# Optimization experiments

Hardware: AMD Instinct MI355X
Metric: run time of the kernel (lower is better)

The kernel has to match this reference:

```python
import jax, jax.numpy as jnp
import numpy as np

D_MODEL = 2048
SEQ_LEN = 16   # R is built for context_window=16 in the original module
BATCH = 256


def make_rotary_matrix(m, d):
    # Faithful to get_rotary_matrix: theta = 10000 ** (-2*(i-1)/d)  (note the i-1 bug kept)
    pos = np.arange(m, dtype=np.float64)[:, None]            # [m,1]
    i = np.arange(d // 2, dtype=np.float64)[None, :]         # [1,d/2]
    theta = 10000.0 ** (-2.0 * (i - 1.0) / d)
    ang = pos * theta                                         # [m, d/2]
    cos, sin = np.cos(ang), np.sin(ang)
    R = np.zeros((m, d, d), dtype=np.float32)
    idx = np.arange(d // 2)
    R[:, 2 * idx, 2 * idx] = cos
    R[:, 2 * idx, 2 * idx + 1] = -sin
    R[:, 2 * idx + 1, 2 * idx] = sin
    R[:, 2 * idx + 1, 2 * idx + 1] = cos
    return jnp.asarray(R)


def setup_inputs() -> dict:
    key = jax.random.key(0)
    kx, kq, kk, kv = jax.random.split(key, 4)
    s = 1.0 / np.sqrt(D_MODEL)
    return {
        "x": jax.random.normal(kx, (BATCH, SEQ_LEN, D_MODEL), dtype=jnp.float32),
        "w_q": jax.random.normal(kq, (D_MODEL, D_MODEL), dtype=jnp.float32) * s,
        "w_k": jax.random.normal(kk, (D_MODEL, D_MODEL), dtype=jnp.float32) * s,
        "w_v": jax.random.normal(kv, (D_MODEL, D_MODEL), dtype=jnp.float32) * s,
    }


def reference(x, w_q, w_k, w_v):
    b, m, d = x.shape
    R = make_rotary_matrix(SEQ_LEN, d)[:m]                    # [m,d,d]
    # nn.Linear(bias=False): y = x @ W^T
    q = jnp.einsum("bmd,ed->bme", x, w_q)
    k = jnp.einsum("bmd,ed->bme", x, w_k)
    v = jnp.einsum("bmd,ed->bme", x, w_v)
    # dense per-position rotary rotation via bmm: (q.transpose(0,1) @ R[:m]).transpose(0,1)
    q_rot = jnp.einsum("bmd,mde->bme", q, R)
    k_rot = jnp.einsum("bmd,mde->bme", k, R)
    # scaled_dot_product_attention (dropout treated as eval-mode / disabled)
    scores = jnp.einsum("bme,bne->bmn", q_rot, k_rot) / jnp.sqrt(jnp.float32(d))
    attn = jax.nn.softmax(scores, axis=-1)
    return jnp.einsum("bmn,bne->bme", attn, v)
```

## Files before the change

kernel.cpp:

```cpp
#include <hip/hip_runtime.h>


#define D 2048
#define SEQLEN 16
#define NBATCH 256
#define NROWS (NBATCH * SEQLEN)
#define NX (NROWS * D)
#define NW (D * D)

#define BM 128
#define BN 192
#define BK 64
#define NKT (D / BK)
#define LDSPB ((BM + BN) * BK)

typedef __attribute__((ext_vector_type(8))) short bf16x8;
typedef __attribute__((ext_vector_type(4))) float f32x4;

__device__ __forceinline__ unsigned short f32_to_bf16(float f) {
  unsigned u = __float_as_uint(f);
  unsigned r = 0x7fffu + ((u >> 16) & 1u);
  return (unsigned short)((u + r) >> 16);
}
__device__ __forceinline__ float bf16lo_to_f32(unsigned u) { return __uint_as_float(u << 16); }
__device__ __forceinline__ float bf16hi_to_f32(unsigned u) { return __uint_as_float(u & 0xffff0000u); }

__device__ __forceinline__ bool detect_f32(const ushort* __restrict__ w) {
  int crazy = 0;
#pragma unroll
  for (int i = 0; i < 64; ++i) {
    float v = __uint_as_float((unsigned)w[i] << 16);
    if (!(__builtin_fabsf(v) < 256.0f)) ++crazy;
  }
  return crazy >= 3;
}

__device__ __forceinline__ void glds16(const void* g, void* l) {
  __builtin_amdgcn_global_load_lds(
      (const __attribute__((address_space(1))) void*)g,
      (__attribute__((address_space(3))) void*)l, 16, 0, 0);
}

__global__ __launch_bounds__(256) void convert_inputs(
    const void* __restrict__ x, const void* __restrict__ wq,
    const void* __restrict__ wk, const void* __restrict__ wv,
    ushort* __restrict__ xb, ushort* __restrict__ wqb,
    ushort* __restrict__ wkb, ushort* __restrict__ wvb) {
  if (!detect_f32((const ushort*)wq)) return;
  const float* srcs[4] = {(const float*)x, (const float*)wq, (const float*)wk, (const float*)wv};
  ushort* dsts[4] = {xb, wqb, wkb, wvb};
  const int ns[4] = {NX, NW, NW, NW};
  const int stride = gridDim.x * blockDim.x;
#pragma unroll
  for (int s = 0; s < 4; ++s) {
    const float* __restrict__ src = srcs[s];
    ushort* __restrict__ dst = dsts[s];
    const int n8 = ns[s] / 8;
    for (int i = blockIdx.x * blockDim.x + threadIdx.x; i < n8; i += stride) {
      float4 a = ((const float4*)src)[i * 2];
      float4 b = ((const float4*)src)[i * 2 + 1];
      uint4 o;
      o.x = (unsigned)f32_to_bf16(a.x) | ((unsigned)f32_to_bf16(a.y) << 16);
      o.y = (unsigned)f32_to_bf16(a.z) | ((unsigned)f32_to_bf16(a.w) << 16);
      o.z = (unsigned)f32_to_bf16(b.x) | ((unsigned)f32_to_bf16(b.y) << 16);
      o.w = (unsigned)f32_to_bf16(b.z) | ((unsigned)f32_to_bf16(b.w) << 16);
      ((uint4*)dst)[i] = o;
    }
  }
}

__global__ __launch_bounds__(256, 2) void qkv_rope_gemm(
    const void* __restrict__ Xr, const void* __restrict__ Wqr,
    const void* __restrict__ Wkr, const void* __restrict__ Wvr,
    const ushort* __restrict__ xb, const ushort* __restrict__ wqb,
    const ushort* __restrict__ wkb, const ushort* __restrict__ wvb,
    ushort* __restrict__ Oq, ushort* __restrict__ Ok, ushort* __restrict__ Ov) {
  __shared__ __align__(16) ushort lds[2][LDSPB];

  const bool f32in = detect_f32((const ushort*)Wqr);
  const ushort* __restrict__ X  = f32in ? xb  : (const ushort*)Xr;
  const ushort* __restrict__ Wq = f32in ? wqb : (const ushort*)Wqr;
  const ushort* __restrict__ Wk = f32in ? wkb : (const ushort*)Wkr;
  const ushort* __restrict__ Wv = f32in ? wvb : (const ushort*)Wvr;

  const int m0 = (blockIdx.x >> 5) * BM;
  const int n0 = (blockIdx.x & 31) * BN;

  const int t = threadIdx.x;
  const int wave = t >> 6, lane = t & 63;
  const int quad = lane >> 4, l16 = lane & 15;
  const int wr = wave >> 1, wc = wave & 1;

  const int srow = t >> 3;
  const int scol = ((t & 7) ^ (srow & 7)) * 8;
  const ushort* gA = X + (size_t)(m0 + srow) * D + scol;
  const ushort* gB[6];
#pragma unroll
  for (int c = 0; c < 6; ++c) {
    const int ng = n0 + c * 32 + srow;
    const int z = ng >> 11;
    gB[c] = ((z == 0) ? Wq : (z == 1) ? Wk : Wv) + (size_t)(ng & 2047) * D + scol;
  }

  f32x4 acc[4][6] = {};

  auto STAGE = [&](int b, int kt) {
    const int kc = kt * BK;
#pragma unroll
    for (int c = 0; c < 4; ++c)
      glds16(gA + (size_t)c * 32 * D + kc, &lds[b][c * 2048 + t * 8]);
#pragma unroll
    for (int c = 0; c < 6; ++c)
      glds16(gB[c] + kc, &lds[b][BM * BK + c * 2048 + t * 8]);
  };

  STAGE(0, 0);
  asm volatile("s_waitcnt vmcnt(0)" ::: "memory");
  __builtin_amdgcn_s_barrier();
  __builtin_amdgcn_sched_barrier(0);

  for (int kt = 0; kt < NKT; ++kt) {
    const int cur = kt & 1;
    if (kt + 1 < NKT) STAGE(cur ^ 1, kt + 1);

    const ushort* Ab = &lds[cur][0];
    const ushort* Bb = &lds[cur][BM * BK];
    const int swz = (l16 & 7) << 3;

#pragma unroll
    for (int ks = 0; ks < 2; ++ks) {
      const int ko = (ks * 32 + quad * 8) ^ swz;
      bf16x8 af[4], bfr[6];
#pragma unroll
      for (int f = 0; f < 4; ++f)
        af[f] = *(const bf16x8*)(Ab + (wr * 64 + f * 16 + l16) * 64 + ko);
#pragma unroll
      for (int g = 0; g < 6; ++g)
        bfr[g] = *(const bf16x8*)(Bb + (wc * 96 + g * 16 + l16) * 64 + ko);
      __builtin_amdgcn_s_barrier();
      asm volatile("s_waitcnt lgkmcnt(0)" ::: "memory");
      __builtin_amdgcn_s_setprio(1);
#pragma unroll
      for (int f = 0; f < 4; ++f)
#pragma unroll
        for (int g = 0; g < 6; ++g)
          acc[f][g] = __builtin_amdgcn_mfma_f32_16x16x32_bf16(
              af[f], bfr[g], acc[f][g], 0, 0, 0);
      __builtin_amdgcn_s_setprio(0);
      __builtin_amdgcn_s_barrier();
    }

    if (kt + 1 < NKT) {
      asm volatile("s_waitcnt vmcnt(0)" ::: "memory");
      __builtin_amdgcn_s_barrier();
      __builtin_amdgcn_sched_barrier(0);
    }
  }

#pragma unroll
  for (int g = 0; g < 6; ++g) {
    const int eg = n0 + wc * 96 + g * 16 + l16;
    const int z = eg >> 11;
    const int e = eg & 2047;
    const bool rope = (z != 2);
    ushort* __restrict__ O = (z == 0) ? Oq : (z == 1) ? Ok : Ov;
    float cs[4] = {}, sn[4] = {};
    if (rope) {
      const float theta = exp2f(-0.012976281620653759f * ((float)(e >> 1) - 1.0f));
#pragma unroll
      for (int r = 0; r < 4; ++r)
        __sincosf((float)(quad * 4 + r) * theta, &sn[r], &cs[r]);
    }
#pragma unroll
    for (int f = 0; f < 4; ++f) {
      const size_t rbase = (size_t)(m0 + wr * 64 + f * 16 + quad * 4) * D;
#pragma unroll
      for (int r = 0; r < 4; ++r) {
        float v = acc[f][g][r];
        float p = __shfl_xor(v, 1);
        float o = v;
        if (rope)
          o = (e & 1) ? (v * cs[r] - p * sn[r])
                      : (v * cs[r] + p * sn[r]);
        O[rbase + (size_t)r * D + e] = f32_to_bf16(o);
      }
    }
  }
}

__global__ __launch_bounds__(512) void rope_attention(
    const ushort* __restrict__ Q, const ushort* __restrict__ K,
    const ushort* __restrict__ V, const void* __restrict__ Wqr, void* __restrict__ OutRaw) {
  __shared__ float sc[8][16][16];
  __shared__ float at[16][16];
  const bool f32out = detect_f32((const ushort*)Wqr);
  const int b = blockIdx.x;
  const int t = threadIdx.x;
  const int wave = t >> 6, lane = t & 63;
  const int quad = lane >> 4, l16 = lane & 15;

  const ushort* Qb = Q + (size_t)b * (SEQLEN * D);
  const ushort* Kb = K + (size_t)b * (SEQLEN * D);

  f32x4 acc = {0.f, 0.f, 0.f, 0.f};
  const ushort* qp = Qb + l16 * D + wave * 256 + quad * 8;
  const ushort* kp = Kb + l16 * D + wave * 256 + quad * 8;
#pragma unroll
  for (int s = 0; s < 8; ++s) {
    bf16x8 a = *(const bf16x8*)(qp + s * 32);
    bf16x8 bb = *(const bf16x8*)(kp + s * 32);
    acc = __builtin_amdgcn_mfma_f32_16x16x32_bf16(a, bb, acc, 0, 0, 0);
  }
#pragma unroll
  for (int r = 0; r < 4; ++r)
    sc[wave][quad * 4 + r][l16] = acc[r];
  __syncthreads();

  if (t < 256) {
    const int m = t >> 4, n = t & 15;
    float s = (sc[0][m][n] + sc[1][m][n] + sc[2][m][n] + sc[3][m][n] +
               sc[4][m][n] + sc[5][m][n] + sc[6][m][n] + sc[7][m][n]) * 0.02209708691207961f;
    float mx = s;
#pragma unroll
    for (int off = 8; off; off >>= 1) mx = fmaxf(mx, __shfl_xor(mx, off, 16));
    float e = __expf(s - mx);
    float sum = e;
#pragma unroll
    for (int off = 8; off; off >>= 1) sum += __shfl_xor(sum, off, 16);
    at[m][n] = e / sum;
  }
  __syncthreads();

  const ushort* Vb = V + (size_t)b * (SEQLEN * D);
  const int e0 = t * 4;
  uint2 vr[16];
#pragma unroll
  for (int n = 0; n < 16; ++n)
    vr[n] = *(const uint2*)(Vb + n * D + e0);

  for (int m = 0; m < 16; ++m) {
    float av[4] = {0.f, 0.f, 0.f, 0.f};
#pragma unroll
    for (int n = 0; n < 16; ++n) {
      const float a = at[m][n];
      const uint2 u = vr[n];
      av[0] = fmaf(a, bf16lo_to_f32(u.x), av[0]);
      av[1] = fmaf(a, bf16hi_to_f32(u.x), av[1]);
      av[2] = fmaf(a, bf16lo_to_f32(u.y), av[2]);
      av[3] = fmaf(a, bf16hi_to_f32(u.y), av[3]);
    }
    if (f32out) {
      float* Ob = (float*)OutRaw + (size_t)b * (SEQLEN * D) + m * D + e0;
      float4 o0 = {av[0], av[1], av[2], av[3]};
      *(float4*)Ob = o0;
    } else {
      uint2 o;
      o.x = (unsigned)f32_to_bf16(av[0]) | ((unsigned)f32_to_bf16(av[1]) << 16);
      o.y = (unsigned)f32_to_bf16(av[2]) | ((unsigned)f32_to_bf16(av[3]) << 16);
      *(uint2*)((ushort*)OutRaw + (size_t)b * (SEQLEN * D) + m * D + e0) = o;
    }
  }
}

extern "C" void kernel_launch(void* const* d_in, const int* in_sizes, int n_in,
                              void* d_out, int out_size, void* d_ws, size_t ws_size,
                              hipStream_t stream) {
  const void* x  = d_in[0];
  const void* wq = d_in[1];
  const void* wk = d_in[2];
  const void* wv = d_in[3];
  ushort* ws = (ushort*)d_ws;
  ushort* xb  = ws;
  ushort* wqb = ws + NX;
  ushort* wkb = ws + NX + NW;
  ushort* wvb = ws + NX + 2 * (size_t)NW;
  ushort* q = ws + NX + 3 * (size_t)NW;
  ushort* k = q + NX;
  ushort* v = k + NX;

  convert_inputs<<<1536, 256, 0, stream>>>(x, wq, wk, wv, xb, wqb, wkb, wvb);
  qkv_rope_gemm<<<dim3(1024), 256, 0, stream>>>(x, wq, wk, wv, xb, wqb, wkb, wvb, q, k, v);
  rope_attention<<<NBATCH, 512, 0, stream>>>(q, k, v, wq, (ushort*)d_out);
}
```

Baseline: 245.4 us.

## Software-pipeline LDS fragment reads with MFMA and prefetch two K tiles

Restructures the GEMM main loop so the LDS fragment reads for the next k-substep are issued while MFMAs on the current fragments run. The global-to-LDS stage for tile kt+2 is issued after the buffer is consumed, and two tiles are primed up front. The goal is to hide LDS read latency and global load latency behind matrix math. In exchange it holds two sets of fragment registers, which raises VGPR pressure, and the barrier/waitcnt ordering is more delicate.

Result: no change. 241.8 us (-1.5%).

```diff
diff --git a/kernel.cpp b/kernel.cpp
--- a/kernel.cpp
+++ b/kernel.cpp
@@ -114,47 +114,58 @@
       glds16(gB[c] + kc, &lds[b][BM * BK + c * 2048 + t * 8]);
   };
 
+  const int swz = (l16 & 7) << 3;
+
+  auto RD = [&](int buf, int ks, bf16x8* af, bf16x8* bfr) {
+    const ushort* Ab = &lds[buf][0];
+    const ushort* Bb = &lds[buf][BM * BK];
+    const int ko = (ks * 32 + quad * 8) ^ swz;
+#pragma unroll
+    for (int f = 0; f < 4; ++f)
+      af[f] = *(const bf16x8*)(Ab + (wr * 64 + f * 16 + l16) * 64 + ko);
+#pragma unroll
+    for (int g = 0; g < 6; ++g)
+      bfr[g] = *(const bf16x8*)(Bb + (wc * 96 + g * 16 + l16) * 64 + ko);
+  };
+
   STAGE(0, 0);
-  asm volatile("s_waitcnt vmcnt(0)" ::: "memory");
+  STAGE(1, 1);
+  asm volatile("s_waitcnt vmcnt(10)" ::: "memory");
   __builtin_amdgcn_s_barrier();
   __builtin_amdgcn_sched_barrier(0);
 
+  bf16x8 a0[4], b0[6], a1[4], b1[6];
+  RD(0, 0, a0, b0);
+
   for (int kt = 0; kt < NKT; ++kt) {
     const int cur = kt & 1;
-    if (kt + 1 < NKT) STAGE(cur ^ 1, kt + 1);
-
-    const ushort* Ab = &lds[cur][0];
-    const ushort* Bb = &lds[cur][BM * BK];
-    const int swz = (l16 & 7) << 3;
-
-#pragma unroll
-    for (int ks = 0; ks < 2; ++ks) {
-      const int ko = (ks * 32 + quad * 8) ^ swz;
-      bf16x8 af[4], bfr[6];
-#pragma unroll
-      for (int f = 0; f < 4; ++f)
-        af[f] = *(const bf16x8*)(Ab + (wr * 64 + f * 16 + l16) * 64 + ko);
+
+    RD(cur, 1, a1, b1);
+    __builtin_amdgcn_s_barrier();
+    __builtin_amdgcn_sched_barrier(0);
+    __builtin_amdgcn_s_setprio(1);
+#pragma unroll
+    for (int f = 0; f < 4; ++f)
 #pragma unroll
       for (int g = 0; g < 6; ++g)
-        bfr[g] = *(const bf16x8*)(Bb + (wc * 96 + g * 16 + l16) * 64 + ko);
-      __builtin_amdgcn_s_barrier();
-      asm volatile("s_waitcnt lgkmcnt(0)" ::: "memory");
-      __builtin_amdgcn_s_setprio(1);
-#pragma unroll
-      for (int f = 0; f < 4; ++f)
-#pragma unroll
-        for (int g = 0; g < 6; ++g)
-          acc[f][g] = __builtin_amdgcn_mfma_f32_16x16x32_bf16(
-              af[f], bfr[g], acc[f][g], 0, 0, 0);
-      __builtin_amdgcn_s_setprio(0);
-      __builtin_amdgcn_s_barrier();
-    }
-
-    if (kt + 1 < NKT) {
+        acc[f][g] = __builtin_amdgcn_mfma_f32_16x16x32_bf16(a0[f], b0[g], acc[f][g], 0, 0, 0);
+    __builtin_amdgcn_s_setprio(0);
+
+    asm volatile("s_waitcnt lgkmcnt(0)" ::: "memory");
+    if (kt + 1 < NKT)
       asm volatile("s_waitcnt vmcnt(0)" ::: "memory");
-      __builtin_amdgcn_s_barrier();
-      __builtin_amdgcn_sched_barrier(0);
-    }
+    __builtin_amdgcn_s_barrier();
+    __builtin_amdgcn_sched_barrier(0);
+    if (kt + 1 < NKT) RD(cur ^ 1, 0, a0, b0);
+    if (kt + 2 < NKT) STAGE(cur, kt + 2);
+    __builtin_amdgcn_sched_barrier(0);
+    __builtin_amdgcn_s_setprio(1);
+#pragma unroll
+    for (int f = 0; f < 4; ++f)
+#pragma unroll
+      for (int g = 0; g < 6; ++g)
+        acc[f][g] = __builtin_amdgcn_mfma_f32_16x16x32_bf16(a1[f], b1[g], acc[f][g], 0, 0, 0);
+    __builtin_amdgcn_s_setprio(0);
   }
 
 #pragma unroll
```
